# Optimization experiments

Measured on AMD Instinct MI355X. Metric: run time of the kernel, lower is better.

The kernel has to match this reference:

```python
import jax, jax.numpy as jnp
import numpy as np

T, B, E, H = 2048, 2, 1024, 16
HD = E // H
L, R = 8, 4
SCALE = HD ** -0.5
NEG = -1e9


def setup_inputs() -> dict:
    key = jax.random.key(0)
    ks = jax.random.split(key, 14)
    c = 0.5  # sqrt(1/rank) constant init for multiplicative factors (fast=True)
    inp = {
        'hidden_states': jax.random.normal(ks[0], (T, B, E), jnp.float32),
        'proj_weight': jax.random.normal(ks[1], (3 * E, E), jnp.float32) * (E ** -0.5),
        'proj_bias': jax.random.normal(ks[2], (3 * E,), jnp.float32) * 0.02,
        'out_weight': jax.random.normal(ks[3], (E, E), jnp.float32) * (E ** -0.5),
        'out_bias': jax.random.normal(ks[4], (E,), jnp.float32) * 0.02,
        'rm_i': c + 0.01 * jax.random.normal(ks[5], (L, R, 3 * E), jnp.float32),
        'sm_i': c + 0.01 * jax.random.normal(ks[6], (L, R, E), jnp.float32),
        'rm_o': c + 0.01 * jax.random.normal(ks[7], (L, R, E), jnp.float32),
        'sm_o': c + 0.01 * jax.random.normal(ks[8], (L, R, E), jnp.float32),
        'r_i': 0.01 * jax.random.normal(ks[9], (L, R, 3 * E), jnp.float32),
        's_i': 0.01 * jax.random.normal(ks[10], (L, R, E), jnp.float32),
        'r_o': 0.01 * jax.random.normal(ks[11], (L, R, E), jnp.float32),
        's_o': 0.01 * jax.random.normal(ks[12], (L, R, E), jnp.float32),
        'lang': jax.random.randint(ks[13], (1,), 0, L, jnp.int32),
    }
    return inp


def reference(hidden_states, proj_weight, proj_bias, out_weight, out_bias,
              rm_i, sm_i, rm_o, sm_o, r_i, s_i, r_o, s_o, lang):
    li = lang[0]
    # multiplicative low-rank modulation (fast_factorize: mm of rank-R factors)
    mul_in = jnp.einsum('re,rf->ef', rm_i[li], sm_i[li])   # [3E, E]
    mul_out = jnp.einsum('re,rf->ef', rm_o[li], sm_o[li])  # [E, E]
    add_in = jnp.einsum('re,rf->ef', r_i[li], s_i[li])
    add_out = jnp.einsum('re,rf->ef', r_o[li], s_o[li])
    w_in = proj_weight * mul_in + add_in    # [3E, E]
    w_out = out_weight * mul_out + add_out  # [E, E]

    # fused QKV projection; rows of w_in are laid out as [H, 3, HD]
    qkv = hidden_states @ w_in.T + proj_bias            # [T, B, 3E]
    qkv = qkv.reshape(T, B, H, 3, HD)
    q = qkv[..., 0, :] * SCALE                          # [T, B, H, HD]
    k = qkv[..., 1, :]
    v = qkv[..., 2, :]

    scores = jnp.einsum('tbhd,sbhd->bhts', q, k)        # [B, H, T, T]
    causal = jnp.tril(jnp.ones((T, T), bool))           # time mask (is_decoder)
    scores = jnp.where(causal, scores, NEG)
    attn = jax.nn.softmax(scores, axis=-1)
    ctx = jnp.einsum('bhts,sbhd->tbhd', attn, v).reshape(T, B, E)
    out = ctx @ w_out.T + out_bias                      # [T, B, E]
    return out
```

## Files before the change

kernel.cpp:

```cpp
#include <hip/hip_runtime.h>
#include <hip/hip_bf16.h>

typedef __attribute__((ext_vector_type(8))) short short8;
typedef __attribute__((ext_vector_type(4))) float f32x4;
typedef unsigned short u16;

#define NEGINF (-1e9f)

__device__ __forceinline__ u16 f2bf(float x) {
    union { float f; unsigned int u; } v; v.f = x;
    unsigned int r = v.u + 0x7fff + ((v.u >> 16) & 1);
    return (u16)(r >> 16);
}

__device__ __forceinline__ float fast_exp2(float x) {
    float r;
    asm volatile("v_exp_f32 %0, %1" : "=v"(r) : "v"(x));
    return r;
}

__device__ __forceinline__ void gload16(const void* g, void* l) {
    __builtin_amdgcn_global_load_lds(
        (const __attribute__((address_space(1))) unsigned int*)g,
        (__attribute__((address_space(3))) unsigned int*)l, 16, 0, 0);
}

__global__ __launch_bounds__(256) void cast_hidden_kernel(const float* __restrict__ in,
                                                          u16* __restrict__ out) {
    int idx = (blockIdx.x * 256 + threadIdx.x) * 4;
    float4 v = *(const float4*)&in[idx];
    ushort4 o;
    o.x = f2bf(v.x); o.y = f2bf(v.y); o.z = f2bf(v.z); o.w = f2bf(v.w);
    *(ushort4*)&out[idx] = o;
}

__global__ __launch_bounds__(256) void prep_w_kernel(const float* __restrict__ w,
                                                     const float* __restrict__ rm,
                                                     const float* __restrict__ sm,
                                                     const float* __restrict__ ra,
                                                     const float* __restrict__ sa,
                                                     const int* __restrict__ lang,
                                                     u16* __restrict__ out, int rows) {
    const int li = lang[0];
    int idx = blockIdx.x * 256 + threadIdx.x;
    int e = idx >> 8;
    int f = (idx & 255) * 4;
    float4 pw = *(const float4*)&w[(size_t)e * 1024 + f];
    float mul0 = 0.f, mul1 = 0.f, mul2 = 0.f, mul3 = 0.f;
    float add0 = 0.f, add1 = 0.f, add2 = 0.f, add3 = 0.f;
#pragma unroll
    for (int r = 0; r < 4; r++) {
        float a = rm[(size_t)(li * 4 + r) * rows + e];
        float4 b = *(const float4*)&sm[(size_t)(li * 4 + r) * 1024 + f];
        float c = ra[(size_t)(li * 4 + r) * rows + e];
        float4 d = *(const float4*)&sa[(size_t)(li * 4 + r) * 1024 + f];
        mul0 += a * b.x; mul1 += a * b.y; mul2 += a * b.z; mul3 += a * b.w;
        add0 += c * d.x; add1 += c * d.y; add2 += c * d.z; add3 += c * d.w;
    }
    ushort4 o;
    o.x = f2bf(pw.x * mul0 + add0);
    o.y = f2bf(pw.y * mul1 + add1);
    o.z = f2bf(pw.z * mul2 + add2);
    o.w = f2bf(pw.w * mul3 + add3);
    *(ushort4*)&out[(size_t)e * 1024 + f] = o;
}

template <int EPI>
__global__ __launch_bounds__(256) void gemm_bf16(const u16* __restrict__ A,
                                                 const u16* __restrict__ W,
                                                 const float* __restrict__ bias,
                                                 int K,
                                                 float* __restrict__ outF,
                                                 u16* __restrict__ qb,
                                                 u16* __restrict__ kb,
                                                 u16* __restrict__ vb) {
    __shared__ __align__(16) u16 As[128 * 32];
    __shared__ __align__(16) u16 Bs[128 * 32];
    const int t = threadIdx.x;
    const int lane = t & 63, wv = t >> 6;
    const int lr = lane & 15, lk = lane >> 4;
    const int wr = wv >> 1, wc = wv & 1;
    const int m0 = blockIdx.y * 128, n0 = blockIdx.x * 128;

    const int rowS = t >> 2, kcS = t & 3;
    const u16* gA0 = A + (size_t)(m0 + rowS) * K + kcS * 8;
    const u16* gA1 = gA0 + (size_t)64 * K;
    const u16* gB0 = W + (size_t)(n0 + rowS) * K + kcS * 8;
    const u16* gB1 = gB0 + (size_t)64 * K;
    char* ldsA0 = (char*)As + wv * 1024;
    char* ldsA1 = (char*)As + 4096 + wv * 1024;
    char* ldsB0 = (char*)Bs + wv * 1024;
    char* ldsB1 = (char*)Bs + 4096 + wv * 1024;

    f32x4 acc[4][4] = {};

    for (int k0 = 0; k0 < K; k0 += 32) {
        gload16(gA0 + k0, ldsA0);
        gload16(gA1 + k0, ldsA1);
        gload16(gB0 + k0, ldsB0);
        gload16(gB1 + k0, ldsB1);
        __syncthreads();
        short8 af[4], bf[4];
#pragma unroll
        for (int mi = 0; mi < 4; mi++)
            af[mi] = *(const short8*)&As[(wr * 64 + mi * 16 + lr) * 32 + lk * 8];
#pragma unroll
        for (int ni = 0; ni < 4; ni++)
            bf[ni] = *(const short8*)&Bs[(wc * 64 + ni * 16 + lr) * 32 + lk * 8];
#pragma unroll
        for (int mi = 0; mi < 4; mi++)
#pragma unroll
            for (int ni = 0; ni < 4; ni++)
                acc[mi][ni] = __builtin_amdgcn_mfma_f32_16x16x32_bf16(af[mi], bf[ni], acc[mi][ni], 0, 0, 0);
        __syncthreads();
    }

#pragma unroll
    for (int mi = 0; mi < 4; mi++) {
#pragma unroll
        for (int ni = 0; ni < 4; ni++) {
            int n = n0 + wc * 64 + ni * 16 + lr;
            float bv = bias[n];
#pragma unroll
            for (int i = 0; i < 4; i++) {
                int m = m0 + wr * 64 + mi * 16 + lk * 4 + i;
                float val = acc[mi][ni][i] + bv;
                if (EPI == 0) {
                    int tt = m >> 1, bb = m & 1;
                    int h = n / 192;
                    int rem = n - h * 192;
                    int s = rem >> 6, d = rem & 63;
                    size_t bh = (size_t)(bb * 16 + h);
                    if (s == 0)      qb[(bh * 2048 + tt) * 64 + d] = f2bf(val * 0.18033688f);
                    else if (s == 1) kb[(bh * 2048 + tt) * 64 + d] = f2bf(val);
                    else             vb[(bh * 2048 + tt) * 64 + d] = f2bf(val);
                } else {
                    outF[(size_t)m * 1024 + n] = val;
                }
            }
        }
    }
}

__global__ __launch_bounds__(256) void tr_v_kernel(const u16* __restrict__ vb,
                                                   u16* __restrict__ vtb) {
    __shared__ u16 tile[64][72];
    const int bh = blockIdx.y;
    const int t0 = blockIdx.x * 64;
    const int tid = threadIdx.x;
    const int row = tid >> 3, c8 = (tid & 7) * 8;
#pragma unroll
    for (int p = 0; p < 2; p++) {
        short8 v = *(const short8*)&vb[((size_t)bh * 2048 + t0 + row + p * 32) * 64 + c8];
        *(short8*)&tile[row + p * 32][c8] = v;
    }
    __syncthreads();
    const int d = tid >> 2, tg = (tid & 3) * 16;
    short8 a, b;
#pragma unroll
    for (int j = 0; j < 8; j++) a[j] = tile[tg + j][d];
#pragma unroll
    for (int j = 0; j < 8; j++) b[j] = tile[tg + 8 + j][d];
    *(short8*)&vtb[((size_t)bh * 64 + d) * 2048 + t0 + tg] = a;
    *(short8*)&vtb[((size_t)bh * 64 + d) * 2048 + t0 + tg + 8] = b;
}

__global__ __launch_bounds__(256) void attn_kernel(const u16* __restrict__ qb,
                                                   const u16* __restrict__ kb,
                                                   const u16* __restrict__ vtb,
                                                   u16* __restrict__ ctx) {
    __shared__ __align__(16) u16 Ks[2][4096];
    __shared__ __align__(16) u16 Vs[2][4096];
    __shared__ __align__(16) u16 Plds[4][16][72];

    const int t = threadIdx.x;
    const int lane = t & 63, wv = t >> 6;
    const int lr = lane & 15, lk = lane >> 4;

    const int d = blockIdx.x;
    const int bh = (d & 7) * 4 + ((d >> 3) >> 4);
    const int pair = (d >> 3) & 15;

    const u16* Kg = kb + (size_t)bh * 2048 * 64;
    const u16* Vg = vtb + (size_t)bh * 64 * 2048;
    const int bb = bh >> 4, h = bh & 15;

    const int p0 = wv * 64 + lane;
    const int r0 = p0 >> 3, c0 = (p0 & 7) ^ (r0 & 7);
    const int p1 = 256 + p0;
    const int r1 = p1 >> 3, c1 = (p1 & 7) ^ (r1 & 7);
    const int ldsOff0 = (wv * 64) * 8;
    const int ldsOff1 = (256 + wv * 64) * 8;

#pragma unroll 1
    for (int sidx = 0; sidx < 2; sidx++) {
        const int strip = sidx == 0 ? pair : 31 - pair;
        const int q0 = strip * 64 + wv * 16;
        const u16* Qp = qb + ((size_t)bh * 2048 + q0) * 64;
        short8 qf0 = *(const short8*)&Qp[lr * 64 + lk * 8];
        short8 qf1 = *(const short8*)&Qp[lr * 64 + 32 + lk * 8];

        f32x4 acc[4] = {};
        float mrow[4], ssum[4];
#pragma unroll
        for (int i = 0; i < 4; i++) { mrow[i] = -3e38f; ssum[i] = 0.f; }

        const int nt = strip + 1;
        int buf = 0;

        {
            gload16(Kg + (size_t)(0 + r0) * 64 + c0 * 8, &Ks[0][ldsOff0]);
            gload16(Kg + (size_t)(0 + r1) * 64 + c1 * 8, &Ks[0][ldsOff1]);
            gload16(Vg + (size_t)r0 * 2048 + 0 + c0 * 8, &Vs[0][ldsOff0]);
            gload16(Vg + (size_t)r1 * 2048 + 0 + c1 * 8, &Vs[0][ldsOff1]);
        }
        asm volatile("s_waitcnt vmcnt(0)" ::: "memory");
        __syncthreads();

#pragma unroll 1
        for (int tt = 0; tt < nt; tt++) {
            const int kv0 = tt * 64;
            if (tt + 1 < nt) {
                const int nkv = kv0 + 64;
                gload16(Kg + (size_t)(nkv + r0) * 64 + c0 * 8, &Ks[buf ^ 1][ldsOff0]);
                gload16(Kg + (size_t)(nkv + r1) * 64 + c1 * 8, &Ks[buf ^ 1][ldsOff1]);
                gload16(Vg + (size_t)r0 * 2048 + nkv + c0 * 8, &Vs[buf ^ 1][ldsOff0]);
                gload16(Vg + (size_t)r1 * 2048 + nkv + c1 * 8, &Vs[buf ^ 1][ldsOff1]);
            }

            f32x4 sb[4];
#pragma unroll
            for (int nj = 0; nj < 4; nj++) {
                const int r = nj * 16 + lr;
                short8 kf0 = *(const short8*)&Ks[buf][r * 64 + ((lk    ) ^ (r & 7)) * 8];
                short8 kf1 = *(const short8*)&Ks[buf][r * 64 + ((lk + 4) ^ (r & 7)) * 8];
                f32x4 z = {0.f, 0.f, 0.f, 0.f};
                z = __builtin_amdgcn_mfma_f32_16x16x32_bf16(qf0, kf0, z, 0, 0, 0);
                z = __builtin_amdgcn_mfma_f32_16x16x32_bf16(qf1, kf1, z, 0, 0, 0);
                sb[nj] = z;
            }
            if (kv0 + 63 > q0) {
#pragma unroll
                for (int nj = 0; nj < 4; nj++) {
                    int kv = kv0 + nj * 16 + lr;
#pragma unroll
                    for (int i = 0; i < 4; i++) {
                        int qr = q0 + lk * 4 + i;
                        if (kv > qr) sb[nj][i] = NEGINF;
                    }
                }
            }
            float scale[4];
#pragma unroll
            for (int i = 0; i < 4; i++) {
                float mx = fmaxf(fmaxf(sb[0][i], sb[1][i]), fmaxf(sb[2][i], sb[3][i]));
                mx = fmaxf(mx, __shfl_xor(mx, 1, 16));
                mx = fmaxf(mx, __shfl_xor(mx, 2, 16));
                mx = fmaxf(mx, __shfl_xor(mx, 4, 16));
                mx = fmaxf(mx, __shfl_xor(mx, 8, 16));
                float mnew = fmaxf(mrow[i], mx);
                scale[i] = fast_exp2(mrow[i] - mnew);
                mrow[i] = mnew;
                float psum = 0.f;
#pragma unroll
                for (int nj = 0; nj < 4; nj++) {
                    float p = fast_exp2(sb[nj][i] - mnew);
                    sb[nj][i] = p;
                    psum += p;
                }
                psum += __shfl_xor(psum, 1, 16);
                psum += __shfl_xor(psum, 2, 16);
                psum += __shfl_xor(psum, 4, 16);
                psum += __shfl_xor(psum, 8, 16);
                ssum[i] = ssum[i] * scale[i] + psum;
            }
#pragma unroll
            for (int nj = 0; nj < 4; nj++)
#pragma unroll
                for (int i = 0; i < 4; i++)
                    Plds[wv][lk * 4 + i][nj * 16 + lr] = f2bf(sb[nj][i]);
#pragma unroll
            for (int ni = 0; ni < 4; ni++)
#pragma unroll
                for (int i = 0; i < 4; i++)
                    acc[ni][i] *= scale[i];
            short8 pf0 = *(const short8*)&Plds[wv][lr][lk * 8];
            short8 pf1 = *(const short8*)&Plds[wv][lr][32 + lk * 8];
#pragma unroll
            for (int ni = 0; ni < 4; ni++) {
                const int r = ni * 16 + lr;
                short8 vf0 = *(const short8*)&Vs[buf][r * 64 + ((lk    ) ^ (r & 7)) * 8];
                short8 vf1 = *(const short8*)&Vs[buf][r * 64 + ((lk + 4) ^ (r & 7)) * 8];
                acc[ni] = __builtin_amdgcn_mfma_f32_16x16x32_bf16(pf0, vf0, acc[ni], 0, 0, 0);
                acc[ni] = __builtin_amdgcn_mfma_f32_16x16x32_bf16(pf1, vf1, acc[ni], 0, 0, 0);
            }

            asm volatile("s_waitcnt vmcnt(0)" ::: "memory");
            __syncthreads();
            buf ^= 1;
        }

#pragma unroll
        for (int ni = 0; ni < 4; ni++) {
#pragma unroll
            for (int i = 0; i < 4; i++) {
                int tq = q0 + lk * 4 + i;
                float val = acc[ni][i] / ssum[i];
                ctx[(size_t)(tq * 2 + bb) * 1024 + h * 64 + ni * 16 + lr] = f2bf(val);
            }
        }
        __syncthreads();
    }
}

extern "C" void kernel_launch(void* const* d_in, const int* in_sizes, int n_in,
                              void* d_out, int out_size, void* d_ws, size_t ws_size,
                              hipStream_t stream) {
    const float* hs     = (const float*)d_in[0];
    const float* proj_w = (const float*)d_in[1];
    const float* proj_b = (const float*)d_in[2];
    const float* out_w  = (const float*)d_in[3];
    const float* out_b  = (const float*)d_in[4];
    const float* rm_i   = (const float*)d_in[5];
    const float* sm_i   = (const float*)d_in[6];
    const float* rm_o   = (const float*)d_in[7];
    const float* sm_o   = (const float*)d_in[8];
    const float* r_i    = (const float*)d_in[9];
    const float* s_i    = (const float*)d_in[10];
    const float* r_o    = (const float*)d_in[11];
    const float* s_o    = (const float*)d_in[12];
    const int*   lang   = (const int*)d_in[13];
    float* out = (float*)d_out;

    char* ws = (char*)d_ws;
    u16* hsb   = (u16*)(ws);
    u16* w_in  = (u16*)(ws + (size_t)(8 << 20));
    u16* w_out = (u16*)(ws + (size_t)(14 << 20));
    u16* qb    = (u16*)(ws + (size_t)(16 << 20));
    u16* kb    = (u16*)(ws + (size_t)(24 << 20));
    u16* vtb   = (u16*)(ws + (size_t)(32 << 20));
    u16* ctxb  = (u16*)(ws + (size_t)(40 << 20));
    u16* vb    = ctxb;

    cast_hidden_kernel<<<dim3(4096), dim3(256), 0, stream>>>(hs, hsb);
    prep_w_kernel<<<dim3(3072), dim3(256), 0, stream>>>(proj_w, rm_i, sm_i, r_i, s_i, lang, w_in, 3072);
    prep_w_kernel<<<dim3(1024), dim3(256), 0, stream>>>(out_w, rm_o, sm_o, r_o, s_o, lang, w_out, 1024);
    gemm_bf16<0><<<dim3(24, 32), dim3(256), 0, stream>>>(hsb, w_in, proj_b, 1024, (float*)nullptr, qb, kb, vb);
    tr_v_kernel<<<dim3(32, 32), dim3(256), 0, stream>>>(vb, vtb);
    attn_kernel<<<dim3(512), dim3(256), 0, stream>>>(qb, kb, vtb, ctxb);
    gemm_bf16<1><<<dim3(8, 32), dim3(256), 0, stream>>>(ctxb, w_out, out_b, 1024, out, (u16*)nullptr, (u16*)nullptr, (u16*)nullptr);
}
```

Measured before the change: 252.7 us.

## Transpose QK^T MFMA so softmax rows are lane-local, skip unneeded rescale

Swaps the QK^T MFMA operands so each lane holds one query row's scores across its four accumulator elements. Row max and sum then need only two cross-lane shuffles per tile, instead of four shuffle steps repeated for each of four rows. The P tile is written to LDS as packed 4-element vectors, and the accumulator rescale is skipped when no row max grew. This cuts shuffle and VALU work in the softmax, but adds per-lane shuffles to redistribute scale and sum values for the output layout.

```diff
diff --git a/kernel.cpp b/kernel.cpp
--- a/kernel.cpp
+++ b/kernel.cpp
@@ -201,9 +201,7 @@
         short8 qf1 = *(const short8*)&Qp[lr * 64 + 32 + lk * 8];
 
         f32x4 acc[4] = {};
-        float mrow[4], ssum[4];
-#pragma unroll
-        for (int i = 0; i < 4; i++) { mrow[i] = -3e38f; ssum[i] = 0.f; }
+        float mrow = -3e38f, ssum = 0.f;
 
         const int nt = strip + 1;
         int buf = 0;
@@ -235,55 +233,65 @@
                 short8 kf0 = *(const short8*)&Ks[buf][r * 64 + ((lk    ) ^ (r & 7)) * 8];
                 short8 kf1 = *(const short8*)&Ks[buf][r * 64 + ((lk + 4) ^ (r & 7)) * 8];
                 f32x4 z = {0.f, 0.f, 0.f, 0.f};
-                z = __builtin_amdgcn_mfma_f32_16x16x32_bf16(qf0, kf0, z, 0, 0, 0);
-                z = __builtin_amdgcn_mfma_f32_16x16x32_bf16(qf1, kf1, z, 0, 0, 0);
+                z = __builtin_amdgcn_mfma_f32_16x16x32_bf16(kf0, qf0, z, 0, 0, 0);
+                z = __builtin_amdgcn_mfma_f32_16x16x32_bf16(kf1, qf1, z, 0, 0, 0);
                 sb[nj] = z;
             }
             if (kv0 + 63 > q0) {
+                const int qr = q0 + lr;
 #pragma unroll
                 for (int nj = 0; nj < 4; nj++) {
-                    int kv = kv0 + nj * 16 + lr;
-#pragma unroll
-                    for (int i = 0; i < 4; i++) {
-                        int qr = q0 + lk * 4 + i;
-                        if (kv > qr) sb[nj][i] = NEGINF;
-                    }
+                    const int kvb = kv0 + nj * 16 + lk * 4;
+#pragma unroll
+                    for (int i = 0; i < 4; i++)
+                        if (kvb + i > qr) sb[nj][i] = NEGINF;
                 }
             }
-            float scale[4];
-#pragma unroll
-            for (int i = 0; i < 4; i++) {
-                float mx = fmaxf(fmaxf(sb[0][i], sb[1][i]), fmaxf(sb[2][i], sb[3][i]));
-                mx = fmaxf(mx, __shfl_xor(mx, 1, 16));
-                mx = fmaxf(mx, __shfl_xor(mx, 2, 16));
-                mx = fmaxf(mx, __shfl_xor(mx, 4, 16));
-                mx = fmaxf(mx, __shfl_xor(mx, 8, 16));
-                float mnew = fmaxf(mrow[i], mx);
-                scale[i] = fast_exp2(mrow[i] - mnew);
-                mrow[i] = mnew;
-                float psum = 0.f;
-#pragma unroll
-                for (int nj = 0; nj < 4; nj++) {
+
+            float pm0 = fmaxf(fmaxf(sb[0][0], sb[0][1]), fmaxf(sb[0][2], sb[0][3]));
+            float pm1 = fmaxf(fmaxf(sb[1][0], sb[1][1]), fmaxf(sb[1][2], sb[1][3]));
+            float pm2 = fmaxf(fmaxf(sb[2][0], sb[2][1]), fmaxf(sb[2][2], sb[2][3]));
+            float pm3 = fmaxf(fmaxf(sb[3][0], sb[3][1]), fmaxf(sb[3][2], sb[3][3]));
+            float pmax = fmaxf(fmaxf(pm0, pm1), fmaxf(pm2, pm3));
+            pmax = fmaxf(pmax, __shfl_xor(pmax, 16));
+            pmax = fmaxf(pmax, __shfl_xor(pmax, 32));
+            const float mold = mrow;
+            const float mnew = fmaxf(mold, pmax);
+            const float scl = fast_exp2(mold - mnew);
+            mrow = mnew;
+            float psum = 0.f;
+#pragma unroll
+            for (int nj = 0; nj < 4; nj++)
+#pragma unroll
+                for (int i = 0; i < 4; i++) {
                     float p = fast_exp2(sb[nj][i] - mnew);
                     sb[nj][i] = p;
                     psum += p;
                 }
-                psum += __shfl_xor(psum, 1, 16);
-                psum += __shfl_xor(psum, 2, 16);
-                psum += __shfl_xor(psum, 4, 16);
-                psum += __shfl_xor(psum, 8, 16);
-                ssum[i] = ssum[i] * scale[i] + psum;
-            }
-#pragma unroll
-            for (int nj = 0; nj < 4; nj++)
-#pragma unroll
-                for (int i = 0; i < 4; i++)
-                    Plds[wv][lk * 4 + i][nj * 16 + lr] = f2bf(sb[nj][i]);
-#pragma unroll
-            for (int ni = 0; ni < 4; ni++)
-#pragma unroll
-                for (int i = 0; i < 4; i++)
-                    acc[ni][i] *= scale[i];
+            psum += __shfl_xor(psum, 16);
+            psum += __shfl_xor(psum, 32);
+            ssum = ssum * scl + psum;
+
+#pragma unroll
+            for (int nj = 0; nj < 4; nj++) {
+                ushort4 pk4;
+                pk4.x = f2bf(sb[nj][0]); pk4.y = f2bf(sb[nj][1]);
+                pk4.z = f2bf(sb[nj][2]); pk4.w = f2bf(sb[nj][3]);
+                *(ushort4*)&Plds[wv][lr][nj * 16 + lk * 4] = pk4;
+            }
+
+            if (!__all(pmax <= mold)) {
+                float s0 = __shfl(scl, lk * 4 + 0);
+                float s1 = __shfl(scl, lk * 4 + 1);
+                float s2 = __shfl(scl, lk * 4 + 2);
+                float s3 = __shfl(scl, lk * 4 + 3);
+#pragma unroll
+                for (int ni = 0; ni < 4; ni++) {
+                    acc[ni][0] *= s0; acc[ni][1] *= s1;
+                    acc[ni][2] *= s2; acc[ni][3] *= s3;
+                }
+            }
+
             short8 pf0 = *(const short8*)&Plds[wv][lr][lk * 8];
             short8 pf1 = *(const short8*)&Plds[wv][lr][32 + lk * 8];
 #pragma unroll
@@ -300,14 +308,18 @@
             buf ^= 1;
         }
 
+        float rs0 = 1.0f / __shfl(ssum, lk * 4 + 0);
+        float rs1 = 1.0f / __shfl(ssum, lk * 4 + 1);
+        float rs2 = 1.0f / __shfl(ssum, lk * 4 + 2);
+        float rs3 = 1.0f / __shfl(ssum, lk * 4 + 3);
 #pragma unroll
         for (int ni = 0; ni < 4; ni++) {
-#pragma unroll
-            for (int i = 0; i < 4; i++) {
-                int tq = q0 + lk * 4 + i;
-                float val = acc[ni][i] / ssum[i];
-                ctx[(size_t)(tq * 2 + bb) * 1024 + h * 64 + ni * 16 + lr] = f2bf(val);
-            }
+            int tq = q0 + lk * 4;
+            int col = h * 64 + ni * 16 + lr;
+            ctx[(size_t)((tq + 0) * 2 + bb) * 1024 + col] = f2bf(acc[ni][0] * rs0);
+            ctx[(size_t)((tq + 1) * 2 + bb) * 1024 + col] = f2bf(acc[ni][1] * rs1);
+            ctx[(size_t)((tq + 2) * 2 + bb) * 1024 + col] = f2bf(acc[ni][2] * rs2);
+            ctx[(size_t)((tq + 3) * 2 + bb) * 1024 + col] = f2bf(acc[ni][3] * rs3);
         }
         __syncthreads();
     }
```

After: 234.7 us. -7.1%, faster.
